# Kernel optimization log

Hardware: AMD Instinct MI355X
Metric: run time of the kernel (lower is better)

The kernel has to match this reference:

```python
import jax, jax.numpy as jnp
import numpy as np

N_NODES = 50000
N_EDGES = 640000
D = 128
BN_EPS = 1e-5


def setup_inputs() -> dict:
    key = jax.random.key(0)
    ks = jax.random.split(key, 12)
    s = 0.05  # weight init scale
    inp = {
        "nh": jax.random.normal(ks[0], (N_NODES, D), jnp.float32),
        "eh": jax.random.normal(ks[1], (N_EDGES, D), jnp.float32),
        "edge_index": jax.random.randint(ks[2], (2, N_EDGES), 0, N_NODES, dtype=jnp.int32),
        # GIN eps parameters (init zeros, as nn.Parameter(torch.zeros(input_dim)))
        "nf_eps": jnp.zeros((D,), jnp.float32),
        "ef_eps": jnp.zeros((D,), jnp.float32),
        # node-feature MLP: Linear(D,D) -> relu -> Linear(D,D)
        "nf_W1": jax.random.normal(ks[3], (D, D), jnp.float32) * s,
        "nf_b1": jnp.zeros((D,), jnp.float32),
        "nf_W2": jax.random.normal(ks[4], (D, D), jnp.float32) * s,
        "nf_b2": jnp.zeros((D,), jnp.float32),
        # edge-feature MLP
        "ef_W1": jax.random.normal(ks[5], (D, D), jnp.float32) * s,
        "ef_b1": jnp.zeros((D,), jnp.float32),
        "ef_W2": jax.random.normal(ks[6], (D, D), jnp.float32) * s,
        "ef_b2": jnp.zeros((D,), jnp.float32),
        # BatchNorm1d affine params (training-mode batch stats)
        "nf_gamma": jnp.ones((D,), jnp.float32),
        "nf_beta": jnp.zeros((D,), jnp.float32),
        "ef_gamma": jnp.ones((D,), jnp.float32),
        "ef_beta": jnp.zeros((D,), jnp.float32),
    }
    return inp


def _mlp(x, W1, b1, W2, b2):
    return jnp.maximum(x @ W1 + b1, 0.0) @ W2 + b2


def _batchnorm(x, gamma, beta):
    # training-mode BatchNorm1d: biased batch variance
    mean = jnp.mean(x, axis=0)
    var = jnp.mean(jnp.square(x - mean), axis=0)
    return (x - mean) * jax.lax.rsqrt(var + BN_EPS) * gamma + beta


def reference(nh, eh, edge_index, nf_eps, ef_eps,
              nf_W1, nf_b1, nf_W2, nf_b2,
              ef_W1, ef_b1, ef_W2, ef_b2,
              nf_gamma, nf_beta, ef_gamma, ef_beta):
    src, dst = edge_index[0], edge_index[1]
    src_nh = nh[src]          # [E, D] gather
    dst_nh = nh[dst]          # [E, D] gather
    msg = src_nh + eh         # [E, D]
    attn = jnp.sum(msg * dst_nh, axis=-1)  # [E]

    # scatter_softmax over destination segments
    seg_max = jax.ops.segment_max(attn, dst, num_segments=N_NODES)  # [N]
    ex = jnp.exp(attn - seg_max[dst])
    seg_sum = jax.ops.segment_sum(ex, dst, num_segments=N_NODES)
    alpha = ex / seg_sum[dst]                                       # [E]

    # scatter_add of weighted source messages
    nz = jax.ops.segment_sum(src_nh * alpha[:, None], dst, num_segments=N_NODES)  # [N, D]

    n_h = (1.0 + nf_eps) * nh + nz
    e_h = (1.0 + ef_eps) * eh + nz[src] - nz[dst]

    n_h = _mlp(n_h, nf_W1, nf_b1, nf_W2, nf_b2)
    e_h = _mlp(e_h, ef_W1, ef_b1, ef_W2, ef_b2)

    n_h = _batchnorm(n_h, nf_gamma, nf_beta)
    e_h = _batchnorm(e_h, ef_gamma, ef_beta)
    return n_h, e_h
```

## Files before the change

### kernel.cpp

```cpp
#include <hip/hip_runtime.h>
#include <cstdint>
#include <cstddef>

#define ND      128
#define NNODES  50000
#define NEDGES  640000
#define BNEPS   1e-5f
#define CAP     64
#define BM      32

typedef __attribute__((ext_vector_type(8))) short bf16x8;
typedef __attribute__((ext_vector_type(4))) short s16x4;
typedef __attribute__((ext_vector_type(4))) float f32x4;

__device__ __forceinline__ short f2bf(float x) {
    unsigned u = __float_as_uint(x);
    unsigned r = u + 0x7fffu + ((u >> 16) & 1u);
    return (short)(r >> 16);
}
__device__ __forceinline__ float bf2f(short h) {
    return __uint_as_float(((unsigned)(unsigned short)h) << 16);
}
__device__ __forceinline__ int swz(int row, int colbyte) {
    return colbyte ^ ((row & 7) << 4);
}

__global__ __launch_bounds__(128) void prep_w_kernel(
    const float* __restrict__ W1, const float* __restrict__ W2,
    short* __restrict__ w1h, short* __restrict__ w1l,
    short* __restrict__ w2h, short* __restrict__ w2l) {
    int k = blockIdx.x;
    int n = threadIdx.x;
    const float* W = (k < 128) ? W1 : W2;
    int kk = k & 127;
    float v = W[(size_t)kk * ND + n];
    short h = f2bf(v);
    short l = f2bf(v - bf2f(h));
    short* ph = (k < 128) ? w1h : w2h;
    short* pl = (k < 128) ? w1l : w2l;
    ph[(size_t)n * ND + kk] = h;
    pl[(size_t)n * ND + kk] = l;
}

__global__ __launch_bounds__(256) void attn_kernel(
    const float* __restrict__ nh, const float* __restrict__ eh,
    const int* __restrict__ ei, float* __restrict__ attn,
    int* __restrict__ deg, int* __restrict__ slots) {
    int gid = blockIdx.x * 256 + threadIdx.x;
    int e   = gid >> 5;
    int l   = threadIdx.x & 31;
    if (e >= NEDGES) return;
    int s = ei[e], d = ei[NEDGES + e];
    float4 sv = ((const float4*)(nh + (size_t)s * ND))[l];
    float4 dv = ((const float4*)(nh + (size_t)d * ND))[l];
    float4 ev = ((const float4*)(eh + (size_t)e * ND))[l];
    float acc = (sv.x + ev.x) * dv.x + (sv.y + ev.y) * dv.y +
                (sv.z + ev.z) * dv.z + (sv.w + ev.w) * dv.w;
#pragma unroll
    for (int off = 16; off > 0; off >>= 1) acc += __shfl_down(acc, off, 32);
    if (l == 0) {
        attn[e] = acc;
        int pos = atomicAdd(&deg[d], 1);
        if (pos < CAP) slots[(size_t)d * CAP + pos] = e;
    }
}

__global__ __launch_bounds__(256) void gather_nz_kernel(
    const float* __restrict__ nh, const int* __restrict__ ei,
    const float* __restrict__ attn, const int* __restrict__ deg,
    const int* __restrict__ slots, float* __restrict__ nz) {
    int node = blockIdx.x * 4 + (threadIdx.x >> 6);
    int lane = threadIdx.x & 63;
    if (node >= NNODES) return;
    int dg = deg[node];
    if (dg > CAP) dg = CAP;

    int   e  = -1, si = 0;
    float a  = -3.0e38f;
    if (lane < dg) {
        e  = slots[(size_t)node * CAP + lane];
        a  = attn[e];
        si = ei[e];
    }
    float m = a;
#pragma unroll
    for (int off = 32; off > 0; off >>= 1) m = fmaxf(m, __shfl_xor(m, off, 64));
    float ex = (lane < dg) ? __expf(a - m) : 0.f;
    float sum = ex;
#pragma unroll
    for (int off = 32; off > 0; off >>= 1) sum += __shfl_xor(sum, off, 64);
    float rs = (dg > 0) ? 1.f / sum : 0.f;

    float2 acc = make_float2(0.f, 0.f);
    for (int i = 0; i < dg; ++i) {
        float al = __shfl(ex, i, 64) * rs;
        int   sv = __shfl(si, i, 64);
        float2 x = ((const float2*)(nh + (size_t)sv * ND))[lane];
        acc.x += al * x.x;
        acc.y += al * x.y;
    }
    ((float2*)(nz + (size_t)node * ND))[lane] = acc;
}

template <int MODE>
__global__ __launch_bounds__(256) void fused_mlp(
    const float* __restrict__ X,
    const short* __restrict__ w1h, const short* __restrict__ w1l,
    const float* __restrict__ b1,
    const short* __restrict__ w2h, const short* __restrict__ w2l,
    float* __restrict__ out, int M,
    const float* __restrict__ eps, const float* __restrict__ nz,
    const int* __restrict__ ei,
    float* __restrict__ ssum, float* __restrict__ ssq) {
    __shared__ short Ah[BM * 128];
    __shared__ short Al[BM * 128];

    int tid  = threadIdx.x;
    int lane = tid & 63;
    int wv   = tid >> 6;
    int cn   = lane & 15;
    int kg   = lane >> 4;
    int row0 = blockIdx.x * BM;
    int cbase = wv * 32;

#pragma unroll
    for (int k = 0; k < BM / 8; ++k) {
        int i   = tid + k * 256;
        int r   = i >> 5;
        int c   = (i & 31) << 2;
        int row = row0 + r;
        float4 v = make_float4(0.f, 0.f, 0.f, 0.f);
        if (MODE == 1 || row < M) {
            float4 xv = *(const float4*)(X + (size_t)row * ND + c);
            float4 e4 = *(const float4*)(eps + c);
            if (MODE == 0) {
                float4 zv = *(const float4*)(nz + (size_t)row * ND + c);
                v.x = (1.f + e4.x) * xv.x + zv.x;
                v.y = (1.f + e4.y) * xv.y + zv.y;
                v.z = (1.f + e4.z) * xv.z + zv.z;
                v.w = (1.f + e4.w) * xv.w + zv.w;
            } else {
                int s = ei[row], d = ei[NEDGES + row];
                float4 zs = *(const float4*)(nz + (size_t)s * ND + c);
                float4 zd = *(const float4*)(nz + (size_t)d * ND + c);
                v.x = (1.f + e4.x) * xv.x + zs.x - zd.x;
                v.y = (1.f + e4.y) * xv.y + zs.y - zd.y;
                v.z = (1.f + e4.z) * xv.z + zs.z - zd.z;
                v.w = (1.f + e4.w) * xv.w + zs.w - zd.w;
            }
        }
        s16x4 hv, lv;
        hv.x = f2bf(v.x); lv.x = f2bf(v.x - bf2f(hv.x));
        hv.y = f2bf(v.y); lv.y = f2bf(v.y - bf2f(hv.y));
        hv.z = f2bf(v.z); lv.z = f2bf(v.z - bf2f(hv.z));
        hv.w = f2bf(v.w); lv.w = f2bf(v.w - bf2f(hv.w));
        int boff = (r << 8) + swz(r, c << 1);
        *(s16x4*)((char*)Ah + boff) = hv;
        *(s16x4*)((char*)Al + boff) = lv;
    }

    bf16x8 bh[2][4], bl[2][4];
#pragma unroll
    for (int cb = 0; cb < 2; ++cb) {
        int n = cbase + cb * 16 + cn;
#pragma unroll
        for (int ks = 0; ks < 4; ++ks) {
            size_t o = (size_t)n * ND + ks * 32 + kg * 8;
            bh[cb][ks] = *(const bf16x8*)(w1h + o);
            bl[cb][ks] = *(const bf16x8*)(w1l + o);
        }
    }
    float b1c[2] = { b1[cbase + cn], b1[cbase + 16 + cn] };

    f32x4 acc[2][2];
#pragma unroll
    for (int rb = 0; rb < 2; ++rb)
#pragma unroll
        for (int cb = 0; cb < 2; ++cb) acc[rb][cb] = (f32x4){0.f, 0.f, 0.f, 0.f};

    __syncthreads();

#pragma unroll
    for (int ks = 0; ks < 4; ++ks) {
        bf16x8 ah[2], al[2];
#pragma unroll
        for (int rb = 0; rb < 2; ++rb) {
            int arow = rb * 16 + cn;
            int aoff = (arow << 8) + swz(arow, (ks << 6) + (kg << 4));
            ah[rb] = *(const bf16x8*)((const char*)Ah + aoff);
            al[rb] = *(const bf16x8*)((const char*)Al + aoff);
        }
#pragma unroll
        for (int rb = 0; rb < 2; ++rb)
#pragma unroll
            for (int cb = 0; cb < 2; ++cb) {
                acc[rb][cb] = __builtin_amdgcn_mfma_f32_16x16x32_bf16(ah[rb], bh[cb][ks], acc[rb][cb], 0, 0, 0);
                acc[rb][cb] = __builtin_amdgcn_mfma_f32_16x16x32_bf16(ah[rb], bl[cb][ks], acc[rb][cb], 0, 0, 0);
                acc[rb][cb] = __builtin_amdgcn_mfma_f32_16x16x32_bf16(al[rb], bh[cb][ks], acc[rb][cb], 0, 0, 0);
            }
    }

    __syncthreads();

#pragma unroll
    for (int cb = 0; cb < 2; ++cb) {
        int n = cbase + cb * 16 + cn;
#pragma unroll
        for (int ks = 0; ks < 4; ++ks) {
            size_t o = (size_t)n * ND + ks * 32 + kg * 8;
            bh[cb][ks] = *(const bf16x8*)(w2h + o);
            bl[cb][ks] = *(const bf16x8*)(w2l + o);
        }
    }

#pragma unroll
    for (int rb = 0; rb < 2; ++rb)
#pragma unroll
        for (int cb = 0; cb < 2; ++cb)
#pragma unroll
            for (int r = 0; r < 4; ++r) {
                float v = acc[rb][cb][r] + b1c[cb];
                v = fmaxf(v, 0.f);
                short h = f2bf(v);
                short l = f2bf(v - bf2f(h));
                int hrow  = rb * 16 + kg * 4 + r;
                int hcolb = (cbase + cb * 16 + cn) << 1;
                int hoff  = (hrow << 8) + swz(hrow, hcolb);
                *(short*)((char*)Ah + hoff) = h;
                *(short*)((char*)Al + hoff) = l;
                acc[rb][cb][r] = 0.f;
            }
    __syncthreads();

#pragma unroll
    for (int ks = 0; ks < 4; ++ks) {
        bf16x8 ah[2], al[2];
#pragma unroll
        for (int rb = 0; rb < 2; ++rb) {
            int arow = rb * 16 + cn;
            int aoff = (arow << 8) + swz(arow, (ks << 6) + (kg << 4));
            ah[rb] = *(const bf16x8*)((const char*)Ah + aoff);
            al[rb] = *(const bf16x8*)((const char*)Al + aoff);
        }
#pragma unroll
        for (int rb = 0; rb < 2; ++rb)
#pragma unroll
            for (int cb = 0; cb < 2; ++cb) {
                acc[rb][cb] = __builtin_amdgcn_mfma_f32_16x16x32_bf16(ah[rb], bh[cb][ks], acc[rb][cb], 0, 0, 0);
                acc[rb][cb] = __builtin_amdgcn_mfma_f32_16x16x32_bf16(ah[rb], bl[cb][ks], acc[rb][cb], 0, 0, 0);
                acc[rb][cb] = __builtin_amdgcn_mfma_f32_16x16x32_bf16(al[rb], bh[cb][ks], acc[rb][cb], 0, 0, 0);
            }
    }

#pragma unroll
    for (int cb = 0; cb < 2; ++cb) {
        int col = cbase + cb * 16 + cn;
        float s = 0.f, s2 = 0.f;
#pragma unroll
        for (int rb = 0; rb < 2; ++rb)
#pragma unroll
            for (int r = 0; r < 4; ++r) {
                float v = acc[rb][cb][r];
                int row = row0 + rb * 16 + kg * 4 + r;
                if (row < M) {
                    out[(size_t)row * ND + col] = v;
                    s += v; s2 += v * v;
                }
            }
        s  += __shfl_down(s, 32, 64);
        s  += __shfl_down(s, 16, 64);
        s2 += __shfl_down(s2, 32, 64);
        s2 += __shfl_down(s2, 16, 64);
        if (kg == 0) {
            unsafeAtomicAdd(&ssum[col], s);
            unsafeAtomicAdd(&ssq[col], s2);
        }
    }
}

__global__ void bn_finalize_kernel(float* __restrict__ sum, float* __restrict__ sumsq,
                                   const float* __restrict__ g, const float* __restrict__ b,
                                   float M) {
    int c = threadIdx.x;
    float mean  = sum[c] / M;
    float var   = sumsq[c] / M - mean * mean;
    float scale = g[c] * rsqrtf(var + BNEPS);
    sum[c]   = scale;
    sumsq[c] = b[c] - mean * scale;
}

__global__ __launch_bounds__(256) void bn_apply_kernel(
    float* __restrict__ x, int M,
    const float* __restrict__ scale, const float* __restrict__ shift) {
    size_t total4 = (size_t)M * (ND / 4);
    for (size_t i = (size_t)blockIdx.x * 256 + threadIdx.x; i < total4;
         i += (size_t)gridDim.x * 256) {
        int c = ((int)(i & 31)) << 2;
        float4 v = ((const float4*)x)[i];
        v.x = v.x * scale[c]     + shift[c];
        v.y = v.y * scale[c + 1] + shift[c + 1];
        v.z = v.z * scale[c + 2] + shift[c + 2];
        v.w = v.w * scale[c + 3] + shift[c + 3];
        ((float4*)x)[i] = v;
    }
}

extern "C" void kernel_launch(void* const* d_in, const int* in_sizes, int n_in,
                              void* d_out, int out_size, void* d_ws, size_t ws_size,
                              hipStream_t stream) {
    const float* nh       = (const float*)d_in[0];
    const float* eh       = (const float*)d_in[1];
    const int*   ei       = (const int*)d_in[2];
    const float* nf_eps   = (const float*)d_in[3];
    const float* ef_eps   = (const float*)d_in[4];
    const float* nf_W1    = (const float*)d_in[5];
    const float* nf_b1    = (const float*)d_in[6];
    const float* nf_W2    = (const float*)d_in[7];
    const float* nf_b2    = (const float*)d_in[8];
    const float* ef_W1    = (const float*)d_in[9];
    const float* ef_b1    = (const float*)d_in[10];
    const float* ef_W2    = (const float*)d_in[11];
    const float* ef_b2    = (const float*)d_in[12];
    const float* nf_gamma = (const float*)d_in[13];
    const float* nf_beta  = (const float*)d_in[14];
    const float* ef_gamma = (const float*)d_in[15];
    const float* ef_beta  = (const float*)d_in[16];

    float* out_n = (float*)d_out;
    float* out_e = (float*)d_out + (size_t)NNODES * ND;

    char* ws = (char*)d_ws;
    size_t off = 0;
    auto alloc = [&](size_t bytes) -> void* {
        void* p = ws + off;
        off = (off + bytes + 255) & ~(size_t)255;
        return p;
    };
    float* attn   = (float*)alloc((size_t)NEDGES * 4);
    float* nz     = (float*)alloc((size_t)NNODES * ND * 4);
    int*   deg    = (int*)alloc((size_t)NNODES * 4);
    int*   slots  = (int*)alloc((size_t)NNODES * CAP * 4);
    float* ssum_n = (float*)alloc(ND * 4);
    float* ssq_n  = (float*)alloc(ND * 4);
    float* ssum_e = (float*)alloc(ND * 4);
    float* ssq_e  = (float*)alloc(ND * 4);
    short* nw1h   = (short*)alloc((size_t)ND * ND * 2);
    short* nw1l   = (short*)alloc((size_t)ND * ND * 2);
    short* nw2h   = (short*)alloc((size_t)ND * ND * 2);
    short* nw2l   = (short*)alloc((size_t)ND * ND * 2);
    short* ew1h   = (short*)alloc((size_t)ND * ND * 2);
    short* ew1l   = (short*)alloc((size_t)ND * ND * 2);
    short* ew2h   = (short*)alloc((size_t)ND * ND * 2);
    short* ew2l   = (short*)alloc((size_t)ND * ND * 2);

    hipMemsetAsync(deg,    0, (size_t)NNODES * 4, stream);
    hipMemsetAsync(ssum_n, 0, ND * 4, stream);
    hipMemsetAsync(ssq_n,  0, ND * 4, stream);
    hipMemsetAsync(ssum_e, 0, ND * 4, stream);
    hipMemsetAsync(ssq_e,  0, ND * 4, stream);

    prep_w_kernel<<<256, 128, 0, stream>>>(nf_W1, nf_W2, nw1h, nw1l, nw2h, nw2l);
    prep_w_kernel<<<256, 128, 0, stream>>>(ef_W1, ef_W2, ew1h, ew1l, ew2h, ew2l);

    attn_kernel<<<NEDGES / 8, 256, 0, stream>>>(nh, eh, ei, attn, deg, slots);
    gather_nz_kernel<<<(NNODES + 3) / 4, 256, 0, stream>>>(nh, ei, attn, deg, slots, nz);

    fused_mlp<0><<<(NNODES + BM - 1) / BM, 256, 0, stream>>>(
        nh, nw1h, nw1l, nf_b1, nw2h, nw2l, out_n, NNODES,
        nf_eps, nz, nullptr, ssum_n, ssq_n);
    fused_mlp<1><<<NEDGES / BM, 256, 0, stream>>>(
        eh, ew1h, ew1l, ef_b1, ew2h, ew2l, out_e, NEDGES,
        ef_eps, nz, ei, ssum_e, ssq_e);

    bn_finalize_kernel<<<1, 128, 0, stream>>>(ssum_n, ssq_n, nf_gamma, nf_beta, (float)NNODES);
    bn_finalize_kernel<<<1, 128, 0, stream>>>(ssum_e, ssq_e, ef_gamma, ef_beta, (float)NEDGES);
    bn_apply_kernel<<<2048, 256, 0, stream>>>(out_n, NNODES, ssum_n, ssq_n);
    bn_apply_kernel<<<8192, 256, 0, stream>>>(out_e, NEDGES, ssum_e, ssq_e);
}
```

Measured before the change: 1.361 ms.

## Retile fused MLP to 64-row blocks with 8 waves and streamed weights

The fused MLP kernel now processes 64 rows per block using 512 threads (8 waves), with each wave owning one 16-column slice instead of two. Instead of holding all weight fragments in registers, each wave loads one k-slice of weights per step and prefetches the next slice. This cuts register pressure so launch_bounds(512,8) can raise occupancy, and it halves the number of blocks and per-block BN atomics. The cost is more weight loads from global/L2 inside the MFMA loop, plus a wasted prefetch on the last iteration.

New measurement: 1.149 ms. 15.6% less time.

```diff
diff --git a/kernel.cpp b/kernel.cpp
--- a/kernel.cpp
+++ b/kernel.cpp
@@ -7,7 +7,7 @@
 #define NEDGES  640000
 #define BNEPS   1e-5f
 #define CAP     64
-#define BM      32
+#define BM      64
 
 typedef __attribute__((ext_vector_type(8))) short bf16x8;
 typedef __attribute__((ext_vector_type(4))) short s16x4;
@@ -103,7 +103,7 @@
 }
 
 template <int MODE>
-__global__ __launch_bounds__(256) void fused_mlp(
+__global__ __launch_bounds__(512, 8) void fused_mlp(
     const float* __restrict__ X,
     const short* __restrict__ w1h, const short* __restrict__ w1l,
     const float* __restrict__ b1,
@@ -121,11 +121,11 @@
     int cn   = lane & 15;
     int kg   = lane >> 4;
     int row0 = blockIdx.x * BM;
-    int cbase = wv * 32;
-
-#pragma unroll
-    for (int k = 0; k < BM / 8; ++k) {
-        int i   = tid + k * 256;
+    int ncol = wv * 16 + cn;
+
+#pragma unroll
+    for (int k = 0; k < BM / 16; ++k) {
+        int i   = tid + k * 512;
         int r   = i >> 5;
         int c   = (i & 31) << 2;
         int row = row0 + r;
@@ -159,111 +159,96 @@
         *(s16x4*)((char*)Al + boff) = lv;
     }
 
-    bf16x8 bh[2][4], bl[2][4];
-#pragma unroll
-    for (int cb = 0; cb < 2; ++cb) {
-        int n = cbase + cb * 16 + cn;
-#pragma unroll
-        for (int ks = 0; ks < 4; ++ks) {
-            size_t o = (size_t)n * ND + ks * 32 + kg * 8;
-            bh[cb][ks] = *(const bf16x8*)(w1h + o);
-            bl[cb][ks] = *(const bf16x8*)(w1l + o);
-        }
-    }
-    float b1c[2] = { b1[cbase + cn], b1[cbase + 16 + cn] };
-
-    f32x4 acc[2][2];
-#pragma unroll
-    for (int rb = 0; rb < 2; ++rb)
-#pragma unroll
-        for (int cb = 0; cb < 2; ++cb) acc[rb][cb] = (f32x4){0.f, 0.f, 0.f, 0.f};
+    float b1c = b1[ncol];
+
+    f32x4 acc[4];
+#pragma unroll
+    for (int rb = 0; rb < 4; ++rb) acc[rb] = (f32x4){0.f, 0.f, 0.f, 0.f};
+
+    bf16x8 bhc = *(const bf16x8*)(w1h + (size_t)ncol * ND + kg * 8);
+    bf16x8 blc = *(const bf16x8*)(w1l + (size_t)ncol * ND + kg * 8);
 
     __syncthreads();
 
 #pragma unroll
     for (int ks = 0; ks < 4; ++ks) {
-        bf16x8 ah[2], al[2];
-#pragma unroll
-        for (int rb = 0; rb < 2; ++rb) {
+        int ksn = (ks + 1) & 3;
+        size_t o = (size_t)ncol * ND + ksn * 32 + kg * 8;
+        bf16x8 bhn = *(const bf16x8*)(w1h + o);
+        bf16x8 bln = *(const bf16x8*)(w1l + o);
+        bf16x8 ah[4], al[4];
+#pragma unroll
+        for (int rb = 0; rb < 4; ++rb) {
             int arow = rb * 16 + cn;
             int aoff = (arow << 8) + swz(arow, (ks << 6) + (kg << 4));
             ah[rb] = *(const bf16x8*)((const char*)Ah + aoff);
             al[rb] = *(const bf16x8*)((const char*)Al + aoff);
         }
 #pragma unroll
-        for (int rb = 0; rb < 2; ++rb)
-#pragma unroll
-            for (int cb = 0; cb < 2; ++cb) {
-                acc[rb][cb] = __builtin_amdgcn_mfma_f32_16x16x32_bf16(ah[rb], bh[cb][ks], acc[rb][cb], 0, 0, 0);
-                acc[rb][cb] = __builtin_amdgcn_mfma_f32_16x16x32_bf16(ah[rb], bl[cb][ks], acc[rb][cb], 0, 0, 0);
-                acc[rb][cb] = __builtin_amdgcn_mfma_f32_16x16x32_bf16(al[rb], bh[cb][ks], acc[rb][cb], 0, 0, 0);
-            }
+        for (int rb = 0; rb < 4; ++rb) {
+            acc[rb] = __builtin_amdgcn_mfma_f32_16x16x32_bf16(ah[rb], bhc, acc[rb], 0, 0, 0);
+            acc[rb] = __builtin_amdgcn_mfma_f32_16x16x32_bf16(ah[rb], blc, acc[rb], 0, 0, 0);
+            acc[rb] = __builtin_amdgcn_mfma_f32_16x16x32_bf16(al[rb], bhc, acc[rb], 0, 0, 0);
+        }
+        bhc = bhn; blc = bln;
     }
 
     __syncthreads();
 
 #pragma unroll
-    for (int cb = 0; cb < 2; ++cb) {
-        int n = cbase + cb * 16 + cn;
-#pragma unroll
-        for (int ks = 0; ks < 4; ++ks) {
-            size_t o = (size_t)n * ND + ks * 32 + kg * 8;
-            bh[cb][ks] = *(const bf16x8*)(w2h + o);
-            bl[cb][ks] = *(const bf16x8*)(w2l + o);
-        }
-    }
-
-#pragma unroll
-    for (int rb = 0; rb < 2; ++rb)
-#pragma unroll
-        for (int cb = 0; cb < 2; ++cb)
-#pragma unroll
-            for (int r = 0; r < 4; ++r) {
-                float v = acc[rb][cb][r] + b1c[cb];
-                v = fmaxf(v, 0.f);
-                short h = f2bf(v);
-                short l = f2bf(v - bf2f(h));
-                int hrow  = rb * 16 + kg * 4 + r;
-                int hcolb = (cbase + cb * 16 + cn) << 1;
-                int hoff  = (hrow << 8) + swz(hrow, hcolb);
-                *(short*)((char*)Ah + hoff) = h;
-                *(short*)((char*)Al + hoff) = l;
-                acc[rb][cb][r] = 0.f;
-            }
+    for (int rb = 0; rb < 4; ++rb)
+#pragma unroll
+        for (int r = 0; r < 4; ++r) {
+            float v = acc[rb][r] + b1c;
+            v = fmaxf(v, 0.f);
+            short h = f2bf(v);
+            short l = f2bf(v - bf2f(h));
+            int hrow  = rb * 16 + kg * 4 + r;
+            int hcolb = ncol << 1;
+            int hoff  = (hrow << 8) + swz(hrow, hcolb);
+            *(short*)((char*)Ah + hoff) = h;
+            *(short*)((char*)Al + hoff) = l;
+            acc[rb][r] = 0.f;
+        }
+
+    bhc = *(const bf16x8*)(w2h + (size_t)ncol * ND + kg * 8);
+    blc = *(const bf16x8*)(w2l + (size_t)ncol * ND + kg * 8);
+
     __syncthreads();
 
 #pragma unroll
     for (int ks = 0; ks < 4; ++ks) {
-        bf16x8 ah[2], al[2];
-#pragma unroll
-        for (int rb = 0; rb < 2; ++rb) {
+        int ksn = (ks + 1) & 3;
+        size_t o = (size_t)ncol * ND + ksn * 32 + kg * 8;
+        bf16x8 bhn = *(const bf16x8*)(w2h + o);
+        bf16x8 bln = *(const bf16x8*)(w2l + o);
+        bf16x8 ah[4], al[4];
+#pragma unroll
+        for (int rb = 0; rb < 4; ++rb) {
             int arow = rb * 16 + cn;
             int aoff = (arow << 8) + swz(arow, (ks << 6) + (kg << 4));
             ah[rb] = *(const bf16x8*)((const char*)Ah + aoff);
             al[rb] = *(const bf16x8*)((const char*)Al + aoff);
         }
 #pragma unroll
-        for (int rb = 0; rb < 2; ++rb)
-#pragma unroll
-            for (int cb = 0; cb < 2; ++cb) {
-                acc[rb][cb] = __builtin_amdgcn_mfma_f32_16x16x32_bf16(ah[rb], bh[cb][ks], acc[rb][cb], 0, 0, 0);
-                acc[rb][cb] = __builtin_amdgcn_mfma_f32_16x16x32_bf16(ah[rb], bl[cb][ks], acc[rb][cb], 0, 0, 0);
-                acc[rb][cb] = __builtin_amdgcn_mfma_f32_16x16x32_bf16(al[rb], bh[cb][ks], acc[rb][cb], 0, 0, 0);
-            }
-    }
-
-#pragma unroll
-    for (int cb = 0; cb < 2; ++cb) {
-        int col = cbase + cb * 16 + cn;
+        for (int rb = 0; rb < 4; ++rb) {
+            acc[rb] = __builtin_amdgcn_mfma_f32_16x16x32_bf16(ah[rb], bhc, acc[rb], 0, 0, 0);
+            acc[rb] = __builtin_amdgcn_mfma_f32_16x16x32_bf16(ah[rb], blc, acc[rb], 0, 0, 0);
+            acc[rb] = __builtin_amdgcn_mfma_f32_16x16x32_bf16(al[rb], bhc, acc[rb], 0, 0, 0);
+        }
+        bhc = bhn; blc = bln;
+    }
+
+    {
         float s = 0.f, s2 = 0.f;
 #pragma unroll
-        for (int rb = 0; rb < 2; ++rb)
+        for (int rb = 0; rb < 4; ++rb)
 #pragma unroll
             for (int r = 0; r < 4; ++r) {
-                float v = acc[rb][cb][r];
+                float v = acc[rb][r];
                 int row = row0 + rb * 16 + kg * 4 + r;
                 if (row < M) {
-                    out[(size_t)row * ND + col] = v;
+                    out[(size_t)row * ND + ncol] = v;
                     s += v; s2 += v * v;
                 }
             }
@@ -272,8 +257,8 @@
         s2 += __shfl_down(s2, 32, 64);
         s2 += __shfl_down(s2, 16, 64);
         if (kg == 0) {
-            unsafeAtomicAdd(&ssum[col], s);
-            unsafeAtomicAdd(&ssq[col], s2);
+            unsafeAtomicAdd(&ssum[ncol], s);
+            unsafeAtomicAdd(&ssq[ncol], s2);
         }
     }
 }
@@ -365,10 +350,10 @@
     attn_kernel<<<NEDGES / 8, 256, 0, stream>>>(nh, eh, ei, attn, deg, slots);
     gather_nz_kernel<<<(NNODES + 3) / 4, 256, 0, stream>>>(nh, ei, attn, deg, slots, nz);
 
-    fused_mlp<0><<<(NNODES + BM - 1) / BM, 256, 0, stream>>>(
+    fused_mlp<0><<<(NNODES + BM - 1) / BM, 512, 0, stream>>>(
         nh, nw1h, nw1l, nf_b1, nw2h, nw2l, out_n, NNODES,
         nf_eps, nz, nullptr, ssum_n, ssq_n);
-    fused_mlp<1><<<NEDGES / BM, 256, 0, stream>>>(
+    fused_mlp<1><<<NEDGES / BM, 512, 0, stream>>>(
         eh, ew1h, ew1l, ef_b1, ew2h, ew2l, out_e, NEDGES,
         ef_eps, nz, ei, ssum_e, ssq_e);
 
```
